# Kernel optimization log

Measured on AMD Instinct MI355X. Metric: run time of the kernel, lower is better.

## Reference

```python
import jax, jax.numpy as jnp
import numpy as np

N, E, G = 100000, 1600000, 64
IN_DIM, EMB, HID, HEADS, OUT = 128, 128, 32, 4, 64
CAT = HID * HEADS  # 128
EPS = 1e-5
SLOPE = 0.2


def gat_conv(x, src, dst, W, a_src, a_dst, bias):
    # x: [N, F_in]; W: [HEADS*HID, F_in]; a_*: [1, HEADS, HID]; bias: [HEADS*HID]
    h = (x @ W.T).reshape(N, HEADS, HID)
    s_src = (h * a_src).sum(-1)  # [N, HEADS]
    s_dst = (h * a_dst).sum(-1)
    e = jax.nn.leaky_relu(s_src[src] + s_dst[dst], SLOPE)  # [Etot, HEADS]
    m = jax.ops.segment_max(e, dst, num_segments=N)
    p = jnp.exp(e - m[dst])
    denom = jax.ops.segment_sum(p, dst, num_segments=N)
    alpha = p / denom[dst]  # softmax over incoming edges per dst node
    out = jax.ops.segment_sum(h[src] * alpha[:, :, None], dst, num_segments=N)
    return out.reshape(N, CAT) + bias


def graph_norm(x, batch, w, b, mean_scale):
    cnt = jax.ops.segment_sum(jnp.ones((N,), x.dtype), batch, num_segments=G)[:, None]
    mean = jax.ops.segment_sum(x, batch, num_segments=G) / cnt  # [G, C]
    sub = x - mean_scale * mean[batch]
    var = jax.ops.segment_sum(sub * sub, batch, num_segments=G) / cnt
    inv = 1.0 / jnp.sqrt(var + EPS)
    return w * sub * inv[batch] + b


def setup_inputs() -> dict:
    key = jax.random.key(0)
    ks = jax.random.split(key, 20)
    g = lambda k, shape, s: jax.random.normal(k, shape, dtype=jnp.float32) * s
    inp = {
        'x': g(ks[0], (N, IN_DIM), 1.0),
        'edge_index': jax.random.randint(ks[1], (2, E), 0, N, dtype=jnp.int64 if jax.config.read('jax_enable_x64') else jnp.int32),
        'batch': jnp.sort(jax.random.randint(ks[2], (N,), 0, G)),
        'enc_w': g(ks[3], (EMB, IN_DIM), 0.08),
        'enc_b': jnp.zeros((EMB,), jnp.float32),
        'w1': g(ks[4], (HEADS * HID, EMB), 0.08),
        'att_src1': g(ks[5], (1, HEADS, HID), 0.15),
        'att_dst1': g(ks[6], (1, HEADS, HID), 0.15),
        'b1': jnp.zeros((CAT,), jnp.float32),
        'n1_w': jnp.ones((CAT,), jnp.float32),
        'n1_b': jnp.zeros((CAT,), jnp.float32),
        'n1_ms': jnp.ones((CAT,), jnp.float32),
        'w2': g(ks[7], (HEADS * HID, CAT), 0.08),
        'att_src2': g(ks[8], (1, HEADS, HID), 0.15),
        'att_dst2': g(ks[9], (1, HEADS, HID), 0.15),
        'b2': jnp.zeros((CAT,), jnp.float32),
        'n2_w': jnp.ones((CAT,), jnp.float32),
        'n2_b': jnp.zeros((CAT,), jnp.float32),
        'n2_ms': jnp.ones((CAT,), jnp.float32),
        'fc_w': g(ks[10], (OUT, CAT), 0.08),
        'fc_b': jnp.zeros((OUT,), jnp.float32),
    }
    return inp


def reference(x, edge_index, batch, enc_w, enc_b, w1, att_src1, att_dst1, b1,
              n1_w, n1_b, n1_ms, w2, att_src2, att_dst2, b2, n2_w, n2_b, n2_ms,
              fc_w, fc_b):
    # PyG GATConv adds self-loops by default
    loops = jnp.arange(N, dtype=edge_index.dtype)
    src = jnp.concatenate([edge_index[0], loops])
    dst = jnp.concatenate([edge_index[1], loops])

    h = x @ enc_w.T + enc_b
    h = jax.nn.elu(gat_conv(h, src, dst, w1, att_src1, att_dst1, b1))
    h = graph_norm(h, batch, n1_w, n1_b, n1_ms)  # dropout = identity (eval)
    h = jax.nn.elu(gat_conv(h, src, dst, w2, att_src2, att_dst2, b2))
    h = graph_norm(h, batch, n2_w, n2_b, n2_ms)
    pooled = jax.ops.segment_max(h, batch, num_segments=G)  # global_max_pool
    return pooled @ fc_w.T + fc_b  # out_dim != 1 -> no sigmoid
```

## Files before the change

### kernel.cpp

```cpp
#include <hip/hip_runtime.h>
#include <hip/hip_bf16.h>

#define SLOPE 0.2f
#define EPS_GN 1e-5f
#define APITCH 136
#define NBUCK 391

typedef __attribute__((ext_vector_type(8))) short bfrag;
typedef __attribute__((ext_vector_type(4))) float ffrag;

__device__ __forceinline__ float lrelu(float v) { return v > 0.f ? v : SLOPE * v; }
__device__ __forceinline__ short f2bs(float v) {
    __hip_bfloat16 h = __float2bfloat16(v);
    return *reinterpret_cast<short*>(&h);
}
__device__ __forceinline__ float blo(unsigned int u) { return __uint_as_float(u << 16); }
__device__ __forceinline__ float bhi(unsigned int u) { return __uint_as_float(u & 0xffff0000u); }

__global__ void prep_weights(const float* __restrict__ enc_w,
                             const float* __restrict__ enc_b,
                             const float* __restrict__ w1,
                             const float* __restrict__ w2,
                             unsigned short* __restrict__ WT1b,
                             unsigned short* __restrict__ WT2b,
                             float* __restrict__ bc1, float* __restrict__ bc2) {
    int c = blockIdx.x;
    int k = threadIdx.x;
    __shared__ float w1row[128];
    w1row[k] = w1[c * 128 + k];
    __syncthreads();
    float acc = 0.f;
    for (int j = 0; j < 128; ++j)
        acc = fmaf(w1row[j], enc_w[j * 128 + k], acc);
    WT1b[c * 128 + k] = (unsigned short)f2bs(acc);
    WT2b[c * 128 + k] = (unsigned short)f2bs(w2[c * 128 + k]);
    if (k == 0) {
        float b = 0.f;
        for (int j = 0; j < 128; ++j) b += w1row[j] * enc_b[j];
        bc1[c] = b;
        bc2[c] = 0.f;
    }
}


__global__ void __launch_bounds__(256) bucket_hist(const int* __restrict__ ei,
                                                   int* __restrict__ bhist, int E, int N) {
    __shared__ int h[NBUCK];
    for (int i = threadIdx.x; i < NBUCK; i += 256) h[i] = 0;
    __syncthreads();
    int base = blockIdx.x * 4096;
#pragma unroll
    for (int s = 0; s < 16; ++s) {
        int e = base + s * 256 + threadIdx.x;
        if (e < E + N) {
            int dst = (e < E) ? ei[E + e] : (e - E);
            atomicAdd(&h[dst >> 8], 1);
        }
    }
    __syncthreads();
    for (int i = threadIdx.x; i < NBUCK; i += 256)
        if (h[i]) atomicAdd(&bhist[i], h[i]);
}

__global__ void bucket_scan(const int* __restrict__ bhist,
                            int* __restrict__ bbase, int* __restrict__ bcur) {
    __shared__ int sh[512];
    int t = threadIdx.x;
    int v = (t < NBUCK) ? bhist[t] : 0;
    sh[t] = v;
    __syncthreads();
    for (int off = 1; off < 512; off <<= 1) {
        int add = (t >= off) ? sh[t - off] : 0;
        __syncthreads();
        sh[t] += add;
        __syncthreads();
    }
    if (t < NBUCK) {
        bbase[t] = sh[t] - v;
        bcur[t] = sh[t] - v;
    }
}

__global__ void __launch_bounds__(256) bucket_scatter(const int* __restrict__ ei,
                                                      int* __restrict__ bcur,
                                                      unsigned int* __restrict__ staging,
                                                      int E, int N) {
    __shared__ int h[NBUCK];
    __shared__ int lb[NBUCK];
    for (int i = threadIdx.x; i < NBUCK; i += 256) h[i] = 0;
    __syncthreads();
    int base = blockIdx.x * 4096;
    int srcv[16], dstv[16];
#pragma unroll
    for (int s = 0; s < 16; ++s) {
        int e = base + s * 256 + threadIdx.x;
        srcv[s] = -1;
        if (e < E + N) {
            srcv[s] = (e < E) ? ei[e] : (e - E);
            dstv[s] = (e < E) ? ei[E + e] : (e - E);
            atomicAdd(&h[dstv[s] >> 8], 1);
        }
    }
    __syncthreads();
    for (int i = threadIdx.x; i < NBUCK; i += 256) {
        int c = h[i];
        lb[i] = c ? atomicAdd(&bcur[i], c) : 0;
        h[i] = 0;
    }
    __syncthreads();
#pragma unroll
    for (int s = 0; s < 16; ++s) {
        if (srcv[s] >= 0) {
            int b = dstv[s] >> 8;
            int slot = atomicAdd(&h[b], 1);
            staging[lb[b] + slot] = ((unsigned int)srcv[s] << 8) | (unsigned int)(dstv[s] & 255);
        }
    }
}

__global__ void __launch_bounds__(256) bucket_finalize(
    const unsigned int* __restrict__ staging,
    const int* __restrict__ bbase, const int* __restrict__ bcur,
    int* __restrict__ rowp, int* __restrict__ esrc, int N, int Etot) {
    int b = blockIdx.x, t = threadIdx.x;
    __shared__ int h[256], sc[256];
    h[t] = 0;
    __syncthreads();
    int s0 = bbase[b], s1 = bcur[b];
    for (int j = s0 + t; j < s1; j += 256)
        atomicAdd(&h[staging[j] & 255], 1);
    __syncthreads();
    int d = h[t];
    sc[t] = d;
    __syncthreads();
    for (int off = 1; off < 256; off <<= 1) {
        int add = (t >= off) ? sc[t - off] : 0;
        __syncthreads();
        sc[t] += add;
        __syncthreads();
    }
    int excl = s0 + sc[t] - d;
    int node = b * 256 + t;
    if (node < N) rowp[node] = excl;
    if (b == 0 && t == 0) rowp[N] = Etot;
    __syncthreads();
    h[t] = excl;
    __syncthreads();
    for (int j = s0 + t; j < s1; j += 256) {
        unsigned int p = staging[j];
        int pos = atomicAdd(&h[p & 255], 1);
        esrc[pos] = (int)(p >> 8);
    }
}

__global__ void __launch_bounds__(256) gemm_mfma(
    const void* __restrict__ Ain, const unsigned short* __restrict__ WTb,
    const float* __restrict__ bias, const float* __restrict__ att_src,
    const float* __restrict__ att_dst, const int* __restrict__ batch,
    const float* __restrict__ Ac, const float* __restrict__ Bc,
    unsigned int* __restrict__ H, float* __restrict__ ssrc, float* __restrict__ sdst, int N) {
    __shared__ short Bsh[128 * APITCH];
    __shared__ short Ash[64 * APITCH];
    __shared__ float asrc_s[128], adst_s[128], bias_s[128];
    int tid = threadIdx.x;
    int base = blockIdx.x * 64;

    for (int idx = tid; idx < 2048; idx += 256) {
        int c = idx >> 4, k8 = (idx & 15) * 8;
        uint4 wv = ((const uint4*)WTb)[idx];
        *(uint4*)&Bsh[c * APITCH + k8] = wv;
    }
    if (Ac == nullptr) {
        const float* A = (const float*)Ain;
        for (int idx = tid; idx < 2048; idx += 256) {
            int nl = idx >> 5, k4 = (idx & 31) * 4;
            int node = base + nl;
            float4 v = make_float4(0.f, 0.f, 0.f, 0.f);
            if (node < N) v = ((const float4*)A)[node * 32 + (idx & 31)];
            *(short4*)&Ash[nl * APITCH + k4] =
                make_short4(f2bs(v.x), f2bs(v.y), f2bs(v.z), f2bs(v.w));
        }
    } else {
        const uint4* A4 = (const uint4*)Ain;
        for (int idx = tid; idx < 1024; idx += 256) {
            int nl = idx >> 4, u4 = idx & 15, k8 = u4 * 8;
            int node = base + nl;
            short o[8] = {0, 0, 0, 0, 0, 0, 0, 0};
            if (node < N) {
                uint4 hb = A4[node * 16 + u4];
                int g = batch[node];
                float4 a0 = *(const float4*)&Ac[g * 128 + k8];
                float4 a1 = *(const float4*)&Ac[g * 128 + k8 + 4];
                float4 b0 = *(const float4*)&Bc[g * 128 + k8];
                float4 b1 = *(const float4*)&Bc[g * 128 + k8 + 4];
                o[0] = f2bs(fmaf(blo(hb.x), a0.x, b0.x));
                o[1] = f2bs(fmaf(bhi(hb.x), a0.y, b0.y));
                o[2] = f2bs(fmaf(blo(hb.y), a0.z, b0.z));
                o[3] = f2bs(fmaf(bhi(hb.y), a0.w, b0.w));
                o[4] = f2bs(fmaf(blo(hb.z), a1.x, b1.x));
                o[5] = f2bs(fmaf(bhi(hb.z), a1.y, b1.y));
                o[6] = f2bs(fmaf(blo(hb.w), a1.z, b1.z));
                o[7] = f2bs(fmaf(bhi(hb.w), a1.w, b1.w));
            }
            *(bfrag*)&Ash[nl * APITCH + k8] = *(bfrag*)o;
        }
    }
    if (tid < 128) {
        asrc_s[tid] = att_src[tid];
        adst_s[tid] = att_dst[tid];
        bias_s[tid] = bias[tid];
    }
    __syncthreads();

    int w = tid >> 6, lane = tid & 63, col = lane & 15, quad = lane >> 4;
    int rowBase = w * 16;

    bfrag afr[4];
#pragma unroll
    for (int s = 0; s < 4; ++s)
        afr[s] = *(const bfrag*)&Ash[(rowBase + col) * APITCH + s * 32 + quad * 8];

    ffrag acc[8];
#pragma unroll
    for (int t = 0; t < 8; ++t) acc[t] = (ffrag){0.f, 0.f, 0.f, 0.f};

#pragma unroll
    for (int t = 0; t < 8; ++t) {
#pragma unroll
        for (int s = 0; s < 4; ++s) {
            bfrag bfr = *(const bfrag*)&Bsh[(t * 16 + col) * APITCH + s * 32 + quad * 8];
            acc[t] = __builtin_amdgcn_mfma_f32_16x16x32_bf16(afr[s], bfr, acc[t], 0, 0, 0);
        }
    }

#pragma unroll
    for (int t = 0; t < 8; ++t) {
        int ch = t * 16 + col;
        float bv = bias_s[ch];
#pragma unroll
        for (int r = 0; r < 4; ++r)
            Ash[(rowBase + quad * 4 + r) * APITCH + ch] = f2bs(acc[t][r] + bv);
    }
    __syncthreads();

    float2 av = make_float2(asrc_s[lane * 2], asrc_s[lane * 2 + 1]);
    float2 dv = make_float2(adst_s[lane * 2], adst_s[lane * 2 + 1]);
    for (int r = 0; r < 16; ++r) {
        int node = base + rowBase + r;
        unsigned int hb = *(const unsigned int*)&Ash[(rowBase + r) * APITCH + lane * 2];
        float hx = blo(hb);
        float hy = bhi(hb);
        float vs = hx * av.x + hy * av.y;
        float vd = hx * dv.x + hy * dv.y;
#pragma unroll
        for (int off = 8; off; off >>= 1) {
            vs += __shfl_xor(vs, off, 16);
            vd += __shfl_xor(vd, off, 16);
        }
        if (node < N) {
            H[node * 64 + lane] = hb;
            if ((lane & 15) == 0) {
                int h = lane >> 4;
                ssrc[node * 4 + h] = vs;
                sdst[node * 4 + h] = vd;
            }
        }
    }
}

__global__ void __launch_bounds__(256) agg_kernel(
    const int* __restrict__ row, const int* __restrict__ esrc,
    const float* __restrict__ ssrc, const float* __restrict__ sdst,
    const uint4* __restrict__ H4, const float* __restrict__ bias,
    uint4* __restrict__ out, int N) {
    int n = (blockIdx.x * 256 + threadIdx.x) >> 6;
    int lane = threadIdx.x & 63;
    if (n >= N) return;
    int slot = lane >> 4, li = lane & 15, head = li >> 2;
    int beg = row[n], end = row[n + 1];
    int last = end - 1;
    float sdh = sdst[n * 4 + head];

    float num[8] = {0.f, 0.f, 0.f, 0.f, 0.f, 0.f, 0.f, 0.f};
    float den = 0.f;
    for (int ebase = beg; ebase < end; ebase += 20) {
        int sv[5];
        float av[5];
        uint4 hv[5];
        bool ok[5];
#pragma unroll
        for (int j = 0; j < 5; ++j) {
            int e = ebase + slot + 4 * j;
            ok[j] = (e < end);
            sv[j] = esrc[min(e, last)];
        }
#pragma unroll
        for (int j = 0; j < 5; ++j) {
            av[j] = ssrc[sv[j] * 4 + head];
            hv[j] = H4[sv[j] * 16 + li];
        }
        __builtin_amdgcn_sched_barrier(0);
#pragma unroll
        for (int j = 0; j < 5; ++j) {
            float al = ok[j] ? __expf(lrelu(av[j] + sdh)) : 0.f;
            den += al;
            num[0] = fmaf(al, blo(hv[j].x), num[0]);
            num[1] = fmaf(al, bhi(hv[j].x), num[1]);
            num[2] = fmaf(al, blo(hv[j].y), num[2]);
            num[3] = fmaf(al, bhi(hv[j].y), num[3]);
            num[4] = fmaf(al, blo(hv[j].z), num[4]);
            num[5] = fmaf(al, bhi(hv[j].z), num[5]);
            num[6] = fmaf(al, blo(hv[j].w), num[6]);
            num[7] = fmaf(al, bhi(hv[j].w), num[7]);
        }
    }
    den += __shfl_xor(den, 16);
    den += __shfl_xor(den, 32);
#pragma unroll
    for (int j = 0; j < 8; ++j) {
        num[j] += __shfl_xor(num[j], 16);
        num[j] += __shfl_xor(num[j], 32);
    }
    if (slot == 0) {
        float rh = 1.f / den;
        int c0 = li * 8;
        unsigned int o[4];
#pragma unroll
        for (int p = 0; p < 4; ++p) {
            float v0 = fmaf(num[2 * p], rh, bias[c0 + 2 * p]);
            float v1 = fmaf(num[2 * p + 1], rh, bias[c0 + 2 * p + 1]);
            v0 = v0 > 0.f ? v0 : __expf(v0) - 1.f;
            v1 = v1 > 0.f ? v1 : __expf(v1) - 1.f;
            o[p] = ((unsigned int)(unsigned short)f2bs(v0)) |
                   (((unsigned int)(unsigned short)f2bs(v1)) << 16);
        }
        out[n * 16 + li] = make_uint4(o[0], o[1], o[2], o[3]);
    }
}

template <int POOL>
__global__ void __launch_bounds__(256) stats_kernel(
    const uint4* __restrict__ X4, const int* __restrict__ batch,
    float* __restrict__ part, int N) {
    __shared__ float red[16][16][9];
    int t = threadIdx.x, u4 = t & 15, rg = t >> 4;
    int base = blockIdx.x * 64;
    int g0 = batch[base];

    float s[2][8] = {}, q[2][8] = {};
    float mx[2][8], mn[2][8];
#pragma unroll
    for (int st = 0; st < 2; ++st)
#pragma unroll
        for (int p = 0; p < 8; ++p) { mx[st][p] = -3e38f; mn[st][p] = 3e38f; }

#pragma unroll
    for (int rr = 0; rr < 4; ++rr) {
        int node = base + rg + rr * 16;
        if (node < N) {
            uint4 hb = X4[node * 16 + u4];
            int st = (batch[node] != g0) ? 1 : 0;
            float vv[8] = {blo(hb.x), bhi(hb.x), blo(hb.y), bhi(hb.y),
                           blo(hb.z), bhi(hb.z), blo(hb.w), bhi(hb.w)};
#pragma unroll
            for (int p = 0; p < 8; ++p) {
                s[st][p] += vv[p];
                q[st][p] += vv[p] * vv[p];
                if (POOL) {
                    mx[st][p] = fmaxf(mx[st][p], vv[p]);
                    mn[st][p] = fminf(mn[st][p], vv[p]);
                }
            }
        }
    }

    int uu = t >> 3, ch = t & 7;
    float rs[2] = {0.f, 0.f}, rq[2] = {0.f, 0.f};
    float rmx[2] = {-3e38f, -3e38f}, rmn[2] = {3e38f, 3e38f};
    for (int st = 0; st < 2; ++st) {
#pragma unroll
        for (int p = 0; p < 8; ++p) red[rg][u4][p] = s[st][p];
        __syncthreads();
        if (t < 128) { float a = 0.f; for (int r2 = 0; r2 < 16; ++r2) a += red[r2][uu][ch]; rs[st] = a; }
        __syncthreads();
#pragma unroll
        for (int p = 0; p < 8; ++p) red[rg][u4][p] = q[st][p];
        __syncthreads();
        if (t < 128) { float a = 0.f; for (int r2 = 0; r2 < 16; ++r2) a += red[r2][uu][ch]; rq[st] = a; }
        __syncthreads();
        if (POOL) {
#pragma unroll
            for (int p = 0; p < 8; ++p) red[rg][u4][p] = mx[st][p];
            __syncthreads();
            if (t < 128) { float a = -3e38f; for (int r2 = 0; r2 < 16; ++r2) a = fmaxf(a, red[r2][uu][ch]); rmx[st] = a; }
            __syncthreads();
#pragma unroll
            for (int p = 0; p < 8; ++p) red[rg][u4][p] = mn[st][p];
            __syncthreads();
            if (t < 128) { float a = 3e38f; for (int r2 = 0; r2 < 16; ++r2) a = fminf(a, red[r2][uu][ch]); rmn[st] = a; }
            __syncthreads();
        }
    }
    if (t < 128) {
        float* pb = part + (size_t)blockIdx.x * 8 * 128;
        pb[0 * 128 + t] = rs[0];
        pb[1 * 128 + t] = rq[0];
        pb[2 * 128 + t] = rs[1];
        pb[3 * 128 + t] = rq[1];
        if (POOL) {
            pb[4 * 128 + t] = rmx[0];
            pb[5 * 128 + t] = rmn[0];
            pb[6 * 128 + t] = rmx[1];
            pb[7 * 128 + t] = rmn[1];
        }
    }
}

template <int POOL>
__global__ void reduce_coef(const float* __restrict__ part,
                            const int* __restrict__ batch, int N,
                            const float* __restrict__ w, const float* __restrict__ b,
                            const float* __restrict__ ms,
                            float* __restrict__ Ac, float* __restrict__ Bc,
                            float* __restrict__ pooled) {
    __shared__ int sh2[2];
    int g = blockIdx.x, c = threadIdx.x;
    if (c < 2) {
        int key = g + c;
        int lo = 0, hi = N;
        while (lo < hi) { int m = (lo + hi) >> 1; if (batch[m] < key) lo = m + 1; else hi = m; }
        sh2[c] = lo;
    }
    __syncthreads();
    int sidx = sh2[0], eidx = sh2[1];
    float cnt = (float)(eidx - sidx);
    if (cnt < 0.5f) {
        if (POOL) pooled[g * 128 + c] = 0.f;
        else { Ac[g * 128 + c] = 0.f; Bc[g * 128 + c] = 0.f; }
        return;
    }
    int b0 = sidx >> 6, b1 = (eidx - 1) >> 6;
    float s = 0.f, q = 0.f, M = -3e38f, m = 3e38f;
    for (int bb = b0; bb <= b1; ++bb) {
        int g0b = batch[bb << 6];
        int qoff;
        bool take;
        if (g0b == g) { qoff = 0; take = true; }
        else {
            int g1b = batch[min((bb << 6) + 63, N - 1)];
            take = (g1b == g);
            qoff = 2;
        }
        if (take) {
            const float* pb = part + (size_t)bb * 8 * 128;
            s += pb[qoff * 128 + c];
            q += pb[(qoff + 1) * 128 + c];
            if (POOL) {
                M = fmaxf(M, pb[(4 + qoff) * 128 + c]);
                m = fminf(m, pb[(5 + qoff) * 128 + c]);
            }
        }
    }
    float mean = s / cnt;
    float msv = ms[c];
    float var = q / cnt - msv * (2.f - msv) * mean * mean;
    var = fmaxf(var, 0.f);
    float inv = rsqrtf(var + EPS_GN);
    float a = w[c] * inv;
    float bb2 = b[c] - msv * mean * a;
    if (POOL) pooled[g * 128 + c] = (a >= 0.f) ? fmaf(a, M, bb2) : fmaf(a, m, bb2);
    else { Ac[g * 128 + c] = a; Bc[g * 128 + c] = bb2; }
}

__global__ void fc_kernel(const float* __restrict__ pooled,
                          const float* __restrict__ fcw,
                          const float* __restrict__ fcb,
                          float* __restrict__ out) {
    int g = blockIdx.x, o = threadIdx.x;
    __shared__ float p[128];
    p[o] = pooled[g * 128 + o];
    p[o + 64] = pooled[g * 128 + 64 + o];
    __syncthreads();
    float acc = fcb[o];
    for (int k = 0; k < 128; ++k)
        acc = fmaf(p[k], fcw[o * 128 + k], acc);
    out[g * 64 + o] = acc;
}

extern "C" void kernel_launch(void* const* d_in, const int* in_sizes, int n_in,
                              void* d_out, int out_size, void* d_ws, size_t ws_size,
                              hipStream_t stream) {
    const float* x     = (const float*)d_in[0];
    const int* ei      = (const int*)d_in[1];
    const int* batch   = (const int*)d_in[2];
    const float* enc_w = (const float*)d_in[3];
    const float* enc_b = (const float*)d_in[4];
    const float* w1    = (const float*)d_in[5];
    const float* as1   = (const float*)d_in[6];
    const float* ad1   = (const float*)d_in[7];
    const float* b1    = (const float*)d_in[8];
    const float* n1w   = (const float*)d_in[9];
    const float* n1b   = (const float*)d_in[10];
    const float* n1ms  = (const float*)d_in[11];
    const float* w2    = (const float*)d_in[12];
    const float* as2   = (const float*)d_in[13];
    const float* ad2   = (const float*)d_in[14];
    const float* b2    = (const float*)d_in[15];
    const float* n2w   = (const float*)d_in[16];
    const float* n2b   = (const float*)d_in[17];
    const float* n2ms  = (const float*)d_in[18];
    const float* fcw   = (const float*)d_in[19];
    const float* fcb   = (const float*)d_in[20];
    float* out = (float*)d_out;

    int N = in_sizes[2];
    int E = in_sizes[1] / 2;
    int Etot = E + N;
    int SB = (N + 63) / 64;

    char* ws = (char*)d_ws;
    size_t off = 0;
    auto take = [&](size_t bytes) {
        char* p = ws + off;
        off = (off + bytes + 255) & ~(size_t)255;
        return p;
    };
    unsigned short* WT1b = (unsigned short*)take(128 * 128 * 2);
    unsigned short* WT2b = (unsigned short*)take(128 * 128 * 2);
    float* bc1 = (float*)take(512);
    float* bc2 = (float*)take(512);
    float* ssrc = (float*)take((size_t)N * 16);
    float* sdst = (float*)take((size_t)N * 16);
    int* rowp   = (int*)take((size_t)(N + 1) * 4);
    int* esrc   = (int*)take((size_t)Etot * 4);
    unsigned int* staging = (unsigned int*)take((size_t)Etot * 4);
    int* bbase  = (int*)take(512 * 4);
    int* bcur   = (int*)take(512 * 4);
    int* bhist  = (int*)take(512 * 4);
    unsigned int* H = (unsigned int*)take((size_t)N * 256);
    unsigned int* AG = (unsigned int*)take((size_t)N * 256);
    float* Ac   = (float*)take(64 * 128 * 4);
    float* Bc   = (float*)take(64 * 128 * 4);
    float* part = (float*)take((size_t)SB * 8 * 128 * 4);
    float* pooled = (float*)take(64 * 128 * 4);
    if (off > ws_size) return;

    int EB = (Etot + 4095) / 4096;

    hipMemsetAsync(bhist, 0, 512 * 4, stream);
    prep_weights<<<128, 128, 0, stream>>>(enc_w, enc_b, w1, w2, WT1b, WT2b, bc1, bc2);

    bucket_hist<<<EB, 256, 0, stream>>>(ei, bhist, E, N);
    bucket_scan<<<1, 512, 0, stream>>>(bhist, bbase, bcur);
    bucket_scatter<<<EB, 256, 0, stream>>>(ei, bcur, staging, E, N);
    bucket_finalize<<<NBUCK, 256, 0, stream>>>(staging, bbase, bcur, rowp, esrc, N, Etot);

    gemm_mfma<<<(N + 63) / 64, 256, 0, stream>>>(x, WT1b, bc1, as1, ad1, batch,
                                                 nullptr, nullptr, H, ssrc, sdst, N);
    agg_kernel<<<(N + 3) / 4, 256, 0, stream>>>(rowp, esrc, ssrc, sdst,
                                                (const uint4*)H, b1, (uint4*)AG, N);
    stats_kernel<0><<<SB, 256, 0, stream>>>((const uint4*)AG, batch, part, N);
    reduce_coef<0><<<64, 128, 0, stream>>>(part, batch, N, n1w, n1b, n1ms, Ac, Bc, nullptr);

    gemm_mfma<<<(N + 63) / 64, 256, 0, stream>>>(AG, WT2b, bc2, as2, ad2, batch,
                                                 Ac, Bc, H, ssrc, sdst, N);
    agg_kernel<<<(N + 3) / 4, 256, 0, stream>>>(rowp, esrc, ssrc, sdst,
                                                (const uint4*)H, b2, (uint4*)AG, N);
    stats_kernel<1><<<SB, 256, 0, stream>>>((const uint4*)AG, batch, part, N);
    reduce_coef<1><<<64, 128, 0, stream>>>(part, batch, N, n2w, n2b, n2ms,
                                           nullptr, nullptr, pooled);

    fc_kernel<<<64, 64, 0, stream>>>(pooled, fcw, fcb, out);
}
```

Baseline: 451.4 us.

## Fuse CSR build and weight prep into one kernel with grid barriers

Replaces the multi-kernel bucketed CSR construction (hist, scan, scatter, finalize) and the weight-prep kernel with a single persistent kernel. It counts node degrees with global atomics, runs a two-level scan, and scatters edges by per-node atomic cursors, with software grid barriers between phases. It also folds the final FC layer into the last reduce_coef kernel. This removes several launches and the staging pass. In exchange it adds heavy global atomic contention on per-node counters, and the barriers can deadlock because 391 blocks are assumed to be co-resident. Edge order within each row also becomes nondeterministic.

```diff
diff --git a/kernel.cpp b/kernel.cpp
--- a/kernel.cpp
+++ b/kernel.cpp
@@ -4,7 +4,6 @@
 #define SLOPE 0.2f
 #define EPS_GN 1e-5f
 #define APITCH 136
-#define NBUCK 391
 
 typedef __attribute__((ext_vector_type(8))) short bfrag;
 typedef __attribute__((ext_vector_type(4))) float ffrag;
@@ -17,120 +16,63 @@
 __device__ __forceinline__ float blo(unsigned int u) { return __uint_as_float(u << 16); }
 __device__ __forceinline__ float bhi(unsigned int u) { return __uint_as_float(u & 0xffff0000u); }
 
-__global__ void prep_weights(const float* __restrict__ enc_w,
-                             const float* __restrict__ enc_b,
-                             const float* __restrict__ w1,
-                             const float* __restrict__ w2,
-                             unsigned short* __restrict__ WT1b,
-                             unsigned short* __restrict__ WT2b,
-                             float* __restrict__ bc1, float* __restrict__ bc2) {
-    int c = blockIdx.x;
-    int k = threadIdx.x;
+__device__ __forceinline__ void gbar(int* bar, int nb) {
+    __syncthreads();
+    if (threadIdx.x == 0) {
+        __threadfence();
+        atomicAdd((unsigned int*)bar, 1u);
+        while (atomicAdd((unsigned int*)bar, 0u) < (unsigned int)nb) {
+            __builtin_amdgcn_s_sleep(2);
+        }
+        __threadfence();
+    }
+    __syncthreads();
+}
+
+__global__ void __launch_bounds__(256) build_all(
+    const int* __restrict__ ei,
+    const float* __restrict__ enc_w, const float* __restrict__ enc_b,
+    const float* __restrict__ w1, const float* __restrict__ w2,
+    unsigned short* __restrict__ WT1b, unsigned short* __restrict__ WT2b,
+    float* __restrict__ bc1, float* __restrict__ bc2,
+    int* __restrict__ deg, int* __restrict__ rowp, int* __restrict__ cur,
+    int* __restrict__ esrc, int* __restrict__ bsum, int* __restrict__ bar,
+    int E, int N) {
     __shared__ float w1row[128];
-    w1row[k] = w1[c * 128 + k];
-    __syncthreads();
-    float acc = 0.f;
-    for (int j = 0; j < 128; ++j)
-        acc = fmaf(w1row[j], enc_w[j * 128 + k], acc);
-    WT1b[c * 128 + k] = (unsigned short)f2bs(acc);
-    WT2b[c * 128 + k] = (unsigned short)f2bs(w2[c * 128 + k]);
-    if (k == 0) {
-        float b = 0.f;
-        for (int j = 0; j < 128; ++j) b += w1row[j] * enc_b[j];
-        bc1[c] = b;
-        bc2[c] = 0.f;
-    }
-}
-
-
-__global__ void __launch_bounds__(256) bucket_hist(const int* __restrict__ ei,
-                                                   int* __restrict__ bhist, int E, int N) {
-    __shared__ int h[NBUCK];
-    for (int i = threadIdx.x; i < NBUCK; i += 256) h[i] = 0;
-    __syncthreads();
-    int base = blockIdx.x * 4096;
-#pragma unroll
-    for (int s = 0; s < 16; ++s) {
-        int e = base + s * 256 + threadIdx.x;
-        if (e < E + N) {
-            int dst = (e < E) ? ei[E + e] : (e - E);
-            atomicAdd(&h[dst >> 8], 1);
-        }
-    }
-    __syncthreads();
-    for (int i = threadIdx.x; i < NBUCK; i += 256)
-        if (h[i]) atomicAdd(&bhist[i], h[i]);
-}
-
-__global__ void bucket_scan(const int* __restrict__ bhist,
-                            int* __restrict__ bbase, int* __restrict__ bcur) {
-    __shared__ int sh[512];
-    int t = threadIdx.x;
-    int v = (t < NBUCK) ? bhist[t] : 0;
-    sh[t] = v;
-    __syncthreads();
-    for (int off = 1; off < 512; off <<= 1) {
-        int add = (t >= off) ? sh[t - off] : 0;
-        __syncthreads();
-        sh[t] += add;
-        __syncthreads();
-    }
-    if (t < NBUCK) {
-        bbase[t] = sh[t] - v;
-        bcur[t] = sh[t] - v;
-    }
-}
-
-__global__ void __launch_bounds__(256) bucket_scatter(const int* __restrict__ ei,
-                                                      int* __restrict__ bcur,
-                                                      unsigned int* __restrict__ staging,
-                                                      int E, int N) {
-    __shared__ int h[NBUCK];
-    __shared__ int lb[NBUCK];
-    for (int i = threadIdx.x; i < NBUCK; i += 256) h[i] = 0;
-    __syncthreads();
-    int base = blockIdx.x * 4096;
-    int srcv[16], dstv[16];
-#pragma unroll
-    for (int s = 0; s < 16; ++s) {
-        int e = base + s * 256 + threadIdx.x;
-        srcv[s] = -1;
-        if (e < E + N) {
-            srcv[s] = (e < E) ? ei[e] : (e - E);
-            dstv[s] = (e < E) ? ei[E + e] : (e - E);
-            atomicAdd(&h[dstv[s] >> 8], 1);
-        }
-    }
-    __syncthreads();
-    for (int i = threadIdx.x; i < NBUCK; i += 256) {
-        int c = h[i];
-        lb[i] = c ? atomicAdd(&bcur[i], c) : 0;
-        h[i] = 0;
-    }
-    __syncthreads();
-#pragma unroll
-    for (int s = 0; s < 16; ++s) {
-        if (srcv[s] >= 0) {
-            int b = dstv[s] >> 8;
-            int slot = atomicAdd(&h[b], 1);
-            staging[lb[b] + slot] = ((unsigned int)srcv[s] << 8) | (unsigned int)(dstv[s] & 255);
-        }
-    }
-}
-
-__global__ void __launch_bounds__(256) bucket_finalize(
-    const unsigned int* __restrict__ staging,
-    const int* __restrict__ bbase, const int* __restrict__ bcur,
-    int* __restrict__ rowp, int* __restrict__ esrc, int N, int Etot) {
-    int b = blockIdx.x, t = threadIdx.x;
-    __shared__ int h[256], sc[256];
-    h[t] = 0;
-    __syncthreads();
-    int s0 = bbase[b], s1 = bcur[b];
-    for (int j = s0 + t; j < s1; j += 256)
-        atomicAdd(&h[staging[j] & 255], 1);
-    __syncthreads();
-    int d = h[t];
+    __shared__ int sc[256];
+    __shared__ int ssum[512];
+    int bid = blockIdx.x, t = threadIdx.x, nb = gridDim.x;
+    int Etot = E + N;
+
+    for (int i = bid * 256 + t; i < N; i += nb * 256) deg[i] = 0;
+    if (bid < 128) {
+        int c = bid;
+        if (t < 128) w1row[t] = w1[c * 128 + t];
+        __syncthreads();
+        if (t < 128) {
+            float acc = 0.f;
+            for (int j = 0; j < 128; ++j)
+                acc = fmaf(w1row[j], enc_w[j * 128 + t], acc);
+            WT1b[c * 128 + t] = (unsigned short)f2bs(acc);
+            WT2b[c * 128 + t] = (unsigned short)f2bs(w2[c * 128 + t]);
+            if (t == 0) {
+                float b = 0.f;
+                for (int j = 0; j < 128; ++j) b += w1row[j] * enc_b[j];
+                bc1[c] = b;
+                bc2[c] = 0.f;
+            }
+        }
+    }
+    gbar(bar + 0, nb);
+
+    for (int e = bid * 256 + t; e < Etot; e += nb * 256) {
+        int dst = (e < E) ? ei[E + e] : (e - E);
+        atomicAdd(&deg[dst], 1);
+    }
+    gbar(bar + 1, nb);
+
+    int node = bid * 256 + t;
+    int d = (node < N) ? deg[node] : 0;
     sc[t] = d;
     __syncthreads();
     for (int off = 1; off < 256; off <<= 1) {
@@ -139,17 +81,42 @@
         sc[t] += add;
         __syncthreads();
     }
-    int excl = s0 + sc[t] - d;
-    int node = b * 256 + t;
-    if (node < N) rowp[node] = excl;
-    if (b == 0 && t == 0) rowp[N] = Etot;
-    __syncthreads();
-    h[t] = excl;
-    __syncthreads();
-    for (int j = s0 + t; j < s1; j += 256) {
-        unsigned int p = staging[j];
-        int pos = atomicAdd(&h[p & 255], 1);
-        esrc[pos] = (int)(p >> 8);
+    if (t == 255) bsum[bid] = sc[255];
+    int excl_local = sc[t] - d;
+    gbar(bar + 2, nb);
+
+    if (bid == 0) {
+        int v0 = (t < nb) ? bsum[t] : 0;
+        int v1 = (t + 256 < nb) ? bsum[t + 256] : 0;
+        ssum[t] = v0;
+        ssum[t + 256] = v1;
+        __syncthreads();
+        for (int off = 1; off < 512; off <<= 1) {
+            int a0 = (t >= off) ? ssum[t - off] : 0;
+            int a1 = (t + 256 >= off) ? ssum[t + 256 - off] : 0;
+            __syncthreads();
+            ssum[t] += a0;
+            ssum[t + 256] += a1;
+            __syncthreads();
+        }
+        if (t < nb) bsum[t] = ssum[t] - v0;
+        if (t + 256 < nb) bsum[t + 256] = ssum[t + 256] - v1;
+    }
+    gbar(bar + 3, nb);
+
+    int rbase = bsum[bid];
+    if (node < N) {
+        rowp[node] = rbase + excl_local;
+        cur[node] = rbase + excl_local;
+    }
+    if (bid == 0 && t == 0) rowp[N] = Etot;
+    gbar(bar + 4, nb);
+
+    for (int e = bid * 256 + t; e < Etot; e += nb * 256) {
+        int src = (e < E) ? ei[e] : (e - E);
+        int dst = (e < E) ? ei[E + e] : (e - E);
+        int pos = atomicAdd(&cur[dst], 1);
+        esrc[pos] = src;
     }
 }
 
@@ -422,8 +389,11 @@
                             const float* __restrict__ w, const float* __restrict__ b,
                             const float* __restrict__ ms,
                             float* __restrict__ Ac, float* __restrict__ Bc,
-                            float* __restrict__ pooled) {
+                            const float* __restrict__ fcw,
+                            const float* __restrict__ fcb,
+                            float* __restrict__ out) {
     __shared__ int sh2[2];
+    __shared__ float prow[128];
     int g = blockIdx.x, c = threadIdx.x;
     if (c < 2) {
         int key = g + c;
@@ -434,57 +404,52 @@
     __syncthreads();
     int sidx = sh2[0], eidx = sh2[1];
     float cnt = (float)(eidx - sidx);
-    if (cnt < 0.5f) {
-        if (POOL) pooled[g * 128 + c] = 0.f;
-        else { Ac[g * 128 + c] = 0.f; Bc[g * 128 + c] = 0.f; }
-        return;
-    }
-    int b0 = sidx >> 6, b1 = (eidx - 1) >> 6;
-    float s = 0.f, q = 0.f, M = -3e38f, m = 3e38f;
-    for (int bb = b0; bb <= b1; ++bb) {
-        int g0b = batch[bb << 6];
-        int qoff;
-        bool take;
-        if (g0b == g) { qoff = 0; take = true; }
-        else {
-            int g1b = batch[min((bb << 6) + 63, N - 1)];
-            take = (g1b == g);
-            qoff = 2;
-        }
-        if (take) {
-            const float* pb = part + (size_t)bb * 8 * 128;
-            s += pb[qoff * 128 + c];
-            q += pb[(qoff + 1) * 128 + c];
-            if (POOL) {
-                M = fmaxf(M, pb[(4 + qoff) * 128 + c]);
-                m = fminf(m, pb[(5 + qoff) * 128 + c]);
+    float pooledv = 0.f, a = 0.f, bb2 = 0.f;
+    if (cnt >= 0.5f) {
+        int b0 = sidx >> 6, b1 = (eidx - 1) >> 6;
+        float s = 0.f, q = 0.f, M = -3e38f, m = 3e38f;
+        for (int bb = b0; bb <= b1; ++bb) {
+            int g0b = batch[bb << 6];
+            int qoff;
+            bool take;
+            if (g0b == g) { qoff = 0; take = true; }
+            else {
+                int g1b = batch[min((bb << 6) + 63, N - 1)];
+                take = (g1b == g);
+                qoff = 2;
             }
-        }
-    }
-    float mean = s / cnt;
-    float msv = ms[c];
-    float var = q / cnt - msv * (2.f - msv) * mean * mean;
-    var = fmaxf(var, 0.f);
-    float inv = rsqrtf(var + EPS_GN);
-    float a = w[c] * inv;
-    float bb2 = b[c] - msv * mean * a;
-    if (POOL) pooled[g * 128 + c] = (a >= 0.f) ? fmaf(a, M, bb2) : fmaf(a, m, bb2);
-    else { Ac[g * 128 + c] = a; Bc[g * 128 + c] = bb2; }
-}
-
-__global__ void fc_kernel(const float* __restrict__ pooled,
-                          const float* __restrict__ fcw,
-                          const float* __restrict__ fcb,
-                          float* __restrict__ out) {
-    int g = blockIdx.x, o = threadIdx.x;
-    __shared__ float p[128];
-    p[o] = pooled[g * 128 + o];
-    p[o + 64] = pooled[g * 128 + 64 + o];
-    __syncthreads();
-    float acc = fcb[o];
-    for (int k = 0; k < 128; ++k)
-        acc = fmaf(p[k], fcw[o * 128 + k], acc);
-    out[g * 64 + o] = acc;
+            if (take) {
+                const float* pb = part + (size_t)bb * 8 * 128;
+                s += pb[qoff * 128 + c];
+                q += pb[(qoff + 1) * 128 + c];
+                if (POOL) {
+                    M = fmaxf(M, pb[(4 + qoff) * 128 + c]);
+                    m = fminf(m, pb[(5 + qoff) * 128 + c]);
+                }
+            }
+        }
+        float mean = s / cnt;
+        float msv = ms[c];
+        float var = q / cnt - msv * (2.f - msv) * mean * mean;
+        var = fmaxf(var, 0.f);
+        float inv = rsqrtf(var + EPS_GN);
+        a = w[c] * inv;
+        bb2 = b[c] - msv * mean * a;
+        if (POOL) pooledv = (a >= 0.f) ? fmaf(a, M, bb2) : fmaf(a, m, bb2);
+    }
+    if (POOL) {
+        prow[c] = pooledv;
+        __syncthreads();
+        if (c < 64) {
+            float acc = fcb[c];
+            for (int k = 0; k < 128; ++k)
+                acc = fmaf(prow[k], fcw[c * 128 + k], acc);
+            out[g * 64 + c] = acc;
+        }
+    } else {
+        Ac[g * 128 + c] = a;
+        Bc[g * 128 + c] = bb2;
+    }
 }
 
 extern "C" void kernel_launch(void* const* d_in, const int* in_sizes, int n_in,
@@ -517,6 +482,7 @@
     int E = in_sizes[1] / 2;
     int Etot = E + N;
     int SB = (N + 63) / 64;
+    int NBK = (N + 255) / 256;
 
     char* ws = (char*)d_ws;
     size_t off = 0;
@@ -533,34 +499,30 @@
     float* sdst = (float*)take((size_t)N * 16);
     int* rowp   = (int*)take((size_t)(N + 1) * 4);
     int* esrc   = (int*)take((size_t)Etot * 4);
-    unsigned int* staging = (unsigned int*)take((size_t)Etot * 4);
-    int* bbase  = (int*)take(512 * 4);
-    int* bcur   = (int*)take(512 * 4);
-    int* bhist  = (int*)take(512 * 4);
+    int* deg    = (int*)take((size_t)N * 4);
+    int* cur    = (int*)take((size_t)N * 4);
+    int* bsum   = (int*)take(512 * 4);
+    int* bar    = (int*)take(8 * 4);
     unsigned int* H = (unsigned int*)take((size_t)N * 256);
     unsigned int* AG = (unsigned int*)take((size_t)N * 256);
     float* Ac   = (float*)take(64 * 128 * 4);
     float* Bc   = (float*)take(64 * 128 * 4);
     float* part = (float*)take((size_t)SB * 8 * 128 * 4);
-    float* pooled = (float*)take(64 * 128 * 4);
     if (off > ws_size) return;
 
-    int EB = (Etot + 4095) / 4096;
-
-    hipMemsetAsync(bhist, 0, 512 * 4, stream);
-    prep_weights<<<128, 128, 0, stream>>>(enc_w, enc_b, w1, w2, WT1b, WT2b, bc1, bc2);
-
-    bucket_hist<<<EB, 256, 0, stream>>>(ei, bhist, E, N);
-    bucket_scan<<<1, 512, 0, stream>>>(bhist, bbase, bcur);
-    bucket_scatter<<<EB, 256, 0, stream>>>(ei, bcur, staging, E, N);
-    bucket_finalize<<<NBUCK, 256, 0, stream>>>(staging, bbase, bcur, rowp, esrc, N, Etot);
+    hipMemsetAsync(bar, 0, 8 * 4, stream);
+
+    build_all<<<NBK, 256, 0, stream>>>(ei, enc_w, enc_b, w1, w2,
+                                       WT1b, WT2b, bc1, bc2,
+                                       deg, rowp, cur, esrc, bsum, bar, E, N);
 
     gemm_mfma<<<(N + 63) / 64, 256, 0, stream>>>(x, WT1b, bc1, as1, ad1, batch,
                                                  nullptr, nullptr, H, ssrc, sdst, N);
     agg_kernel<<<(N + 3) / 4, 256, 0, stream>>>(rowp, esrc, ssrc, sdst,
                                                 (const uint4*)H, b1, (uint4*)AG, N);
     stats_kernel<0><<<SB, 256, 0, stream>>>((const uint4*)AG, batch, part, N);
-    reduce_coef<0><<<64, 128, 0, stream>>>(part, batch, N, n1w, n1b, n1ms, Ac, Bc, nullptr);
+    reduce_coef<0><<<64, 128, 0, stream>>>(part, batch, N, n1w, n1b, n1ms, Ac, Bc,
+                                           nullptr, nullptr, nullptr);
 
     gemm_mfma<<<(N + 63) / 64, 256, 0, stream>>>(AG, WT2b, bc2, as2, ad2, batch,
                                                  Ac, Bc, H, ssrc, sdst, N);
@@ -568,7 +530,5 @@
                                                 (const uint4*)H, b2, (uint4*)AG, N);
     stats_kernel<1><<<SB, 256, 0, stream>>>((const uint4*)AG, batch, part, N);
     reduce_coef<1><<<64, 128, 0, stream>>>(part, batch, N, n2w, n2b, n2ms,
-                                           nullptr, nullptr, pooled);
-
-    fc_kernel<<<64, 64, 0, stream>>>(pooled, fcw, fcb, out);
-}
+                                           nullptr, nullptr, fcw, fcb, out);
+}
```

Result: slower. 751.8 us (+66.6%).

## Fuse small setup and reduction kernels into neighbors to cut launches

Applied to the files above, without the earlier changes.

Weight preparation moves into the bucket histogram kernel, which uses its first 128 blocks. The first graph-norm coefficient reduction moves into the second GEMM, where each block recomputes coefficients for at most two graphs from the partial sums. The final reduction is fused with the FC layer. Together these remove three kernel launches and the intermediate Ac/Bc/pooled buffers. In exchange, every GEMM block now redundantly does binary searches and partial-sum reductions, and it assumes a 64-node tile spans no more than two graphs.

```diff
diff --git a/kernel.cpp b/kernel.cpp
--- a/kernel.cpp
+++ b/kernel.cpp
@@ -17,48 +17,44 @@
 __device__ __forceinline__ float blo(unsigned int u) { return __uint_as_float(u << 16); }
 __device__ __forceinline__ float bhi(unsigned int u) { return __uint_as_float(u & 0xffff0000u); }
 
-__global__ void prep_weights(const float* __restrict__ enc_w,
-                             const float* __restrict__ enc_b,
-                             const float* __restrict__ w1,
-                             const float* __restrict__ w2,
-                             unsigned short* __restrict__ WT1b,
-                             unsigned short* __restrict__ WT2b,
-                             float* __restrict__ bc1, float* __restrict__ bc2) {
-    int c = blockIdx.x;
-    int k = threadIdx.x;
+
+__global__ void __launch_bounds__(256) bucket_hist(
+    const int* __restrict__ ei, int* __restrict__ bhist,
+    const float* __restrict__ enc_w, const float* __restrict__ enc_b,
+    const float* __restrict__ w1, const float* __restrict__ w2,
+    unsigned short* __restrict__ WT1b, unsigned short* __restrict__ WT2b,
+    float* __restrict__ bc1, float* __restrict__ bc2, int E, int N) {
+    __shared__ int h[NBUCK];
     __shared__ float w1row[128];
-    w1row[k] = w1[c * 128 + k];
-    __syncthreads();
-    float acc = 0.f;
-    for (int j = 0; j < 128; ++j)
-        acc = fmaf(w1row[j], enc_w[j * 128 + k], acc);
-    WT1b[c * 128 + k] = (unsigned short)f2bs(acc);
-    WT2b[c * 128 + k] = (unsigned short)f2bs(w2[c * 128 + k]);
-    if (k == 0) {
-        float b = 0.f;
-        for (int j = 0; j < 128; ++j) b += w1row[j] * enc_b[j];
-        bc1[c] = b;
-        bc2[c] = 0.f;
-    }
-}
-
-
-__global__ void __launch_bounds__(256) bucket_hist(const int* __restrict__ ei,
-                                                   int* __restrict__ bhist, int E, int N) {
-    __shared__ int h[NBUCK];
-    for (int i = threadIdx.x; i < NBUCK; i += 256) h[i] = 0;
-    __syncthreads();
-    int base = blockIdx.x * 4096;
+    int t = threadIdx.x, bid = blockIdx.x;
+    for (int i = t; i < NBUCK; i += 256) h[i] = 0;
+    bool prep = (bid < 128) && (t < 128);
+    if (prep) w1row[t] = w1[bid * 128 + t];
+    __syncthreads();
+    int base = bid * 4096;
 #pragma unroll
     for (int s = 0; s < 16; ++s) {
-        int e = base + s * 256 + threadIdx.x;
+        int e = base + s * 256 + t;
         if (e < E + N) {
             int dst = (e < E) ? ei[E + e] : (e - E);
             atomicAdd(&h[dst >> 8], 1);
         }
     }
-    __syncthreads();
-    for (int i = threadIdx.x; i < NBUCK; i += 256)
+    if (prep) {
+        float acc = 0.f;
+        for (int j = 0; j < 128; ++j)
+            acc = fmaf(w1row[j], enc_w[j * 128 + t], acc);
+        WT1b[bid * 128 + t] = (unsigned short)f2bs(acc);
+        WT2b[bid * 128 + t] = (unsigned short)f2bs(w2[bid * 128 + t]);
+        if (t == 0) {
+            float b = 0.f;
+            for (int j = 0; j < 128; ++j) b += w1row[j] * enc_b[j];
+            bc1[bid] = b;
+            bc2[bid] = 0.f;
+        }
+    }
+    __syncthreads();
+    for (int i = t; i < NBUCK; i += 256)
         if (h[i]) atomicAdd(&bhist[i], h[i]);
 }
 
@@ -157,11 +153,14 @@
     const void* __restrict__ Ain, const unsigned short* __restrict__ WTb,
     const float* __restrict__ bias, const float* __restrict__ att_src,
     const float* __restrict__ att_dst, const int* __restrict__ batch,
-    const float* __restrict__ Ac, const float* __restrict__ Bc,
+    const float* __restrict__ part, const float* __restrict__ nw,
+    const float* __restrict__ nb_, const float* __restrict__ nms,
     unsigned int* __restrict__ H, float* __restrict__ ssrc, float* __restrict__ sdst, int N) {
     __shared__ short Bsh[128 * APITCH];
     __shared__ short Ash[64 * APITCH];
     __shared__ float asrc_s[128], adst_s[128], bias_s[128];
+    __shared__ float AcS[2][128], BcS[2][128];
+    __shared__ int gse[4];
     int tid = threadIdx.x;
     int base = blockIdx.x * 64;
 
@@ -170,7 +169,7 @@
         uint4 wv = ((const uint4*)WTb)[idx];
         *(uint4*)&Bsh[c * APITCH + k8] = wv;
     }
-    if (Ac == nullptr) {
+    if (part == nullptr) {
         const float* A = (const float*)Ain;
         for (int idx = tid; idx < 2048; idx += 256) {
             int nl = idx >> 5, k4 = (idx & 31) * 4;
@@ -181,6 +180,53 @@
                 make_short4(f2bs(v.x), f2bs(v.y), f2bs(v.z), f2bs(v.w));
         }
     } else {
+        int gA = batch[base];
+        int gB = batch[min(base + 63, N - 1)];
+        if (tid < 4) {
+            int gq = (tid < 2) ? gA : gB;
+            int key = gq + (tid & 1);
+            int lo = 0, hi = N;
+            while (lo < hi) { int m = (lo + hi) >> 1; if (batch[m] < key) lo = m + 1; else hi = m; }
+            gse[tid] = lo;
+        }
+        __syncthreads();
+        {
+            int gi = tid >> 7, c = tid & 127;
+            int g = gi ? gB : gA;
+            int sidx = gse[gi * 2], eidx = gse[gi * 2 + 1];
+            float a = 0.f, bb2 = 0.f;
+            if (eidx > sidx) {
+                int b0 = sidx >> 6, b1 = (eidx - 1) >> 6;
+                float s = 0.f, q = 0.f;
+                for (int bb = b0; bb <= b1; ++bb) {
+                    int g0b = batch[bb << 6];
+                    int qoff;
+                    bool take;
+                    if (g0b == g) { qoff = 0; take = true; }
+                    else {
+                        int g1b = batch[min((bb << 6) + 63, N - 1)];
+                        take = (g1b == g);
+                        qoff = 2;
+                    }
+                    if (take) {
+                        const float* pb = part + (size_t)bb * 8 * 128;
+                        s += pb[qoff * 128 + c];
+                        q += pb[(qoff + 1) * 128 + c];
+                    }
+                }
+                float cnt = (float)(eidx - sidx);
+                float mean = s / cnt;
+                float msv = nms[c];
+                float var = q / cnt - msv * (2.f - msv) * mean * mean;
+                var = fmaxf(var, 0.f);
+                float inv = rsqrtf(var + EPS_GN);
+                a = nw[c] * inv;
+                bb2 = nb_[c] - msv * mean * a;
+            }
+            AcS[gi][c] = a;
+            BcS[gi][c] = bb2;
+        }
+        __syncthreads();
         const uint4* A4 = (const uint4*)Ain;
         for (int idx = tid; idx < 1024; idx += 256) {
             int nl = idx >> 4, u4 = idx & 15, k8 = u4 * 8;
@@ -188,11 +234,11 @@
             short o[8] = {0, 0, 0, 0, 0, 0, 0, 0};
             if (node < N) {
                 uint4 hb = A4[node * 16 + u4];
-                int g = batch[node];
-                float4 a0 = *(const float4*)&Ac[g * 128 + k8];
-                float4 a1 = *(const float4*)&Ac[g * 128 + k8 + 4];
-                float4 b0 = *(const float4*)&Bc[g * 128 + k8];
-                float4 b1 = *(const float4*)&Bc[g * 128 + k8 + 4];
+                int st = (batch[node] != batch[base]) ? 1 : 0;
+                float4 a0 = *(const float4*)&AcS[st][k8];
+                float4 a1 = *(const float4*)&AcS[st][k8 + 4];
+                float4 b0 = *(const float4*)&BcS[st][k8];
+                float4 b1 = *(const float4*)&BcS[st][k8 + 4];
                 o[0] = f2bs(fmaf(blo(hb.x), a0.x, b0.x));
                 o[1] = f2bs(fmaf(bhi(hb.x), a0.y, b0.y));
                 o[2] = f2bs(fmaf(blo(hb.y), a0.z, b0.z));
@@ -416,14 +462,15 @@
     }
 }
 
-template <int POOL>
-__global__ void reduce_coef(const float* __restrict__ part,
-                            const int* __restrict__ batch, int N,
-                            const float* __restrict__ w, const float* __restrict__ b,
-                            const float* __restrict__ ms,
-                            float* __restrict__ Ac, float* __restrict__ Bc,
-                            float* __restrict__ pooled) {
+__global__ void rc_fc(const float* __restrict__ part,
+                      const int* __restrict__ batch, int N,
+                      const float* __restrict__ w, const float* __restrict__ b,
+                      const float* __restrict__ ms,
+                      const float* __restrict__ fcw,
+                      const float* __restrict__ fcb,
+                      float* __restrict__ out) {
     __shared__ int sh2[2];
+    __shared__ float prow[128];
     int g = blockIdx.x, c = threadIdx.x;
     if (c < 2) {
         int key = g + c;
@@ -434,57 +481,45 @@
     __syncthreads();
     int sidx = sh2[0], eidx = sh2[1];
     float cnt = (float)(eidx - sidx);
-    if (cnt < 0.5f) {
-        if (POOL) pooled[g * 128 + c] = 0.f;
-        else { Ac[g * 128 + c] = 0.f; Bc[g * 128 + c] = 0.f; }
-        return;
-    }
-    int b0 = sidx >> 6, b1 = (eidx - 1) >> 6;
-    float s = 0.f, q = 0.f, M = -3e38f, m = 3e38f;
-    for (int bb = b0; bb <= b1; ++bb) {
-        int g0b = batch[bb << 6];
-        int qoff;
-        bool take;
-        if (g0b == g) { qoff = 0; take = true; }
-        else {
-            int g1b = batch[min((bb << 6) + 63, N - 1)];
-            take = (g1b == g);
-            qoff = 2;
-        }
-        if (take) {
-            const float* pb = part + (size_t)bb * 8 * 128;
-            s += pb[qoff * 128 + c];
-            q += pb[(qoff + 1) * 128 + c];
-            if (POOL) {
+    float pooledv = 0.f;
+    if (cnt >= 0.5f) {
+        int b0 = sidx >> 6, b1 = (eidx - 1) >> 6;
+        float s = 0.f, q = 0.f, M = -3e38f, m = 3e38f;
+        for (int bb = b0; bb <= b1; ++bb) {
+            int g0b = batch[bb << 6];
+            int qoff;
+            bool take;
+            if (g0b == g) { qoff = 0; take = true; }
+            else {
+                int g1b = batch[min((bb << 6) + 63, N - 1)];
+                take = (g1b == g);
+                qoff = 2;
+            }
+            if (take) {
+                const float* pb = part + (size_t)bb * 8 * 128;
+                s += pb[qoff * 128 + c];
+                q += pb[(qoff + 1) * 128 + c];
                 M = fmaxf(M, pb[(4 + qoff) * 128 + c]);
                 m = fminf(m, pb[(5 + qoff) * 128 + c]);
             }
         }
-    }
-    float mean = s / cnt;
-    float msv = ms[c];
-    float var = q / cnt - msv * (2.f - msv) * mean * mean;
-    var = fmaxf(var, 0.f);
-    float inv = rsqrtf(var + EPS_GN);
-    float a = w[c] * inv;
-    float bb2 = b[c] - msv * mean * a;
-    if (POOL) pooled[g * 128 + c] = (a >= 0.f) ? fmaf(a, M, bb2) : fmaf(a, m, bb2);
-    else { Ac[g * 128 + c] = a; Bc[g * 128 + c] = bb2; }
-}
-
-__global__ void fc_kernel(const float* __restrict__ pooled,
-                          const float* __restrict__ fcw,
-                          const float* __restrict__ fcb,
-                          float* __restrict__ out) {
-    int g = blockIdx.x, o = threadIdx.x;
-    __shared__ float p[128];
-    p[o] = pooled[g * 128 + o];
-    p[o + 64] = pooled[g * 128 + 64 + o];
-    __syncthreads();
-    float acc = fcb[o];
-    for (int k = 0; k < 128; ++k)
-        acc = fmaf(p[k], fcw[o * 128 + k], acc);
-    out[g * 64 + o] = acc;
+        float mean = s / cnt;
+        float msv = ms[c];
+        float var = q / cnt - msv * (2.f - msv) * mean * mean;
+        var = fmaxf(var, 0.f);
+        float inv = rsqrtf(var + EPS_GN);
+        float a = w[c] * inv;
+        float bb2 = b[c] - msv * mean * a;
+        pooledv = (a >= 0.f) ? fmaf(a, M, bb2) : fmaf(a, m, bb2);
+    }
+    prow[c] = pooledv;
+    __syncthreads();
+    if (c < 64) {
+        float acc = fcb[c];
+        for (int k = 0; k < 128; ++k)
+            acc = fmaf(prow[k], fcw[c * 128 + k], acc);
+        out[g * 64 + c] = acc;
+    }
 }
 
 extern "C" void kernel_launch(void* const* d_in, const int* in_sizes, int n_in,
@@ -539,36 +574,31 @@
     int* bhist  = (int*)take(512 * 4);
     unsigned int* H = (unsigned int*)take((size_t)N * 256);
     unsigned int* AG = (unsigned int*)take((size_t)N * 256);
-    float* Ac   = (float*)take(64 * 128 * 4);
-    float* Bc   = (float*)take(64 * 128 * 4);
     float* part = (float*)take((size_t)SB * 8 * 128 * 4);
-    float* pooled = (float*)take(64 * 128 * 4);
     if (off > ws_size) return;
 
     int EB = (Etot + 4095) / 4096;
 
     hipMemsetAsync(bhist, 0, 512 * 4, stream);
-    prep_weights<<<128, 128, 0, stream>>>(enc_w, enc_b, w1, w2, WT1b, WT2b, bc1, bc2);
-
-    bucket_hist<<<EB, 256, 0, stream>>>(ei, bhist, E, N);
+
+    bucket_hist<<<EB, 256, 0, stream>>>(ei, bhist, enc_w, enc_b, w1, w2,
+                                        WT1b, WT2b, bc1, bc2, E, N);
     bucket_scan<<<1, 512, 0, stream>>>(bhist, bbase, bcur);
     bucket_scatter<<<EB, 256, 0, stream>>>(ei, bcur, staging, E, N);
     bucket_finalize<<<NBUCK, 256, 0, stream>>>(staging, bbase, bcur, rowp, esrc, N, Etot);
 
     gemm_mfma<<<(N + 63) / 64, 256, 0, stream>>>(x, WT1b, bc1, as1, ad1, batch,
-                                                 nullptr, nullptr, H, ssrc, sdst, N);
+                                                 nullptr, nullptr, nullptr, nullptr,
+                                                 H, ssrc, sdst, N);
     agg_kernel<<<(N + 3) / 4, 256, 0, stream>>>(rowp, esrc, ssrc, sdst,
                                                 (const uint4*)H, b1, (uint4*)AG, N);
     stats_kernel<0><<<SB, 256, 0, stream>>>((const uint4*)AG, batch, part, N);
-    reduce_coef<0><<<64, 128, 0, stream>>>(part, batch, N, n1w, n1b, n1ms, Ac, Bc, nullptr);
 
     gemm_mfma<<<(N + 63) / 64, 256, 0, stream>>>(AG, WT2b, bc2, as2, ad2, batch,
-                                                 Ac, Bc, H, ssrc, sdst, N);
+                                                 part, n1w, n1b, n1ms,
+                                                 H, ssrc, sdst, N);
     agg_kernel<<<(N + 3) / 4, 256, 0, stream>>>(rowp, esrc, ssrc, sdst,
                                                 (const uint4*)H, b2, (uint4*)AG, N);
     stats_kernel<1><<<SB, 256, 0, stream>>>((const uint4*)AG, batch, part, N);
-    reduce_coef<1><<<64, 128, 0, stream>>>(part, batch, N, n2w, n2b, n2ms,
-                                           nullptr, nullptr, pooled);
-
-    fc_kernel<<<64, 64, 0, stream>>>(pooled, fcw, fcb, out);
-}
+    rc_fc<<<64, 128, 0, stream>>>(part, batch, N, n2w, n2b, n2ms, fcw, fcb, out);
+}
```

Result: slower. 494.8 us (+9.6%).
